# Kernel tuning notes

Measured on AMD Instinct MI355X. Metric: run time of the kernel, lower is better.

## Reference

```python
import jax, jax.numpy as jnp
import numpy as np

T = 1024
HID = 2880
H = 64        # query heads
KVH = 8       # kv heads
G = H // KVH  # GQA group size
D = 64        # head dim
WIN = 128     # sliding window
BASE = 150000.0
INIT_CTX = 4096
SCALING = 32.0
NTK_ALPHA = 1.0
NTK_BETA = 32.0
EPS = 1e-5


def _rope_cache():
    # YaRN-style NTK rope cache (scaling_factor > 1 branch), computed in float32.
    d_half = D // 2
    freq = BASE ** (np.arange(0, D, 2, dtype=np.float64) / D)
    concentration = 0.1 * np.log(SCALING) + 1.0
    low = d_half * np.log(INIT_CTX / (NTK_BETA * 2 * np.pi)) / np.log(BASE)
    high = d_half * np.log(INIT_CTX / (NTK_ALPHA * 2 * np.pi)) / np.log(BASE)
    interpolation = 1.0 / (SCALING * freq)
    extrapolation = 1.0 / freq
    ramp = (np.arange(d_half, dtype=np.float64) - low) / (high - low)
    mask = 1.0 - np.clip(ramp, 0.0, 1.0)
    inv_freq = interpolation * (1.0 - mask) + extrapolation * mask
    t = np.arange(INIT_CTX, dtype=np.float64)
    freqs = np.outer(t, inv_freq)                  # [INIT_CTX, D/2]
    cos = (np.cos(freqs) * concentration).astype(np.float32)
    sin = (np.sin(freqs) * concentration).astype(np.float32)
    return jnp.asarray(cos), jnp.asarray(sin)

_COS, _SIN = _rope_cache()


def _apply_rope(x, cos, sin):
    # x: [T, nh, D], cos/sin: [T, D/2]
    c = cos[:, None, :]
    s = sin[:, None, :]
    x1, x2 = jnp.split(x, 2, axis=-1)
    return jnp.concatenate([x1 * c - x2 * s, x2 * c + x1 * s], axis=-1)


def setup_inputs() -> dict:
    key = jax.random.key(0)
    ks = jax.random.split(key, 8)
    hidden_states = jax.random.normal(ks[0], (T, HID), dtype=jnp.float32)
    positions = jnp.arange(T, dtype=jnp.int32)
    norm_scale = jnp.ones((HID,), dtype=jnp.float32)
    qkv_out = H * D + 2 * KVH * D  # 4096 + 512 + 512
    w_qkv = jax.random.normal(ks[1], (HID, qkv_out), dtype=jnp.float32) * (HID ** -0.5)
    b_qkv = jax.random.normal(ks[2], (qkv_out,), dtype=jnp.float32) * 0.01
    w_out = jax.random.normal(ks[3], (H * D, HID), dtype=jnp.float32) * ((H * D) ** -0.5)
    b_out = jax.random.normal(ks[4], (HID,), dtype=jnp.float32) * 0.01
    sinks = jax.random.normal(ks[5], (H,), dtype=jnp.float32)
    return {"hidden_states": hidden_states, "positions": positions,
            "norm_scale": norm_scale, "w_qkv": w_qkv, "b_qkv": b_qkv,
            "w_out": w_out, "b_out": b_out, "sinks": sinks}


def reference(hidden_states, positions, norm_scale, w_qkv, b_qkv, w_out, b_out, sinks):
    # RMSNorm (fp32 math)
    t = hidden_states
    t = t * jax.lax.rsqrt(jnp.mean(t * t, axis=-1, keepdims=True) + EPS)
    t = t * norm_scale

    # fused QKV projection
    qkv = t @ w_qkv + b_qkv
    q = qkv[:, : H * D].reshape(T, H, D)
    k = qkv[:, H * D: H * D + KVH * D].reshape(T, KVH, D)
    v = qkv[:, H * D + KVH * D:].reshape(T, KVH, D)

    # RoPE
    cos = _COS[positions]
    sin = _SIN[positions]
    q = _apply_rope(q, cos, sin)
    k = _apply_rope(k, cos, sin)

    # GQA attention with sliding window + learned sinks
    qg = q.reshape(T, KVH, G, D)
    scale = D ** -0.5
    scores = jnp.einsum('qhgd,khd->hgqk', qg, k) * scale  # [KVH, G, T, T]
    i = jnp.arange(T)[:, None]
    j = jnp.arange(T)[None, :]
    allowed = (j <= i) & (j > i - WIN)  # causal + sliding window
    scores = jnp.where(allowed, scores, -jnp.inf)
    sink = sinks.reshape(KVH, G)[..., None]  # [KVH, G, 1]
    lse = jnp.logaddexp(jax.nn.logsumexp(scores, axis=-1), sink)  # [KVH, G, T]
    probs = jnp.exp(scores - lse[..., None])  # sink mass not attached to any value
    attn = jnp.einsum('hgqk,khd->qhgd', probs, v).reshape(T, H * D)

    out = attn @ w_out + b_out
    return out + hidden_states
```

## Files before the change

### kernel.cpp

```cpp
#include <hip/hip_runtime.h>
#include <hip/hip_bf16.h>
#include <math.h>

#define T_SEQ 1024
#define HIDD 2880
#define NH   64
#define NKVH 8
#define GQ   8
#define HD   64
#define WIN  128
#define QKV_N 5120
#define QDIM  4096
#define KOFF  4096
#define VOFF  4608
#define NPAD_OUT 3072
#define RMS_EPS 1e-5f
#define Z1 3
#define KS1 960
#define Z2 4
#define KS2 1024
#define P1SZ (T_SEQ * QKV_N)
#define P2SZ (T_SEQ * HIDD)

typedef __attribute__((ext_vector_type(8))) short short8;
typedef __attribute__((ext_vector_type(4))) short s16x4;
typedef __attribute__((ext_vector_type(4))) float floatx4;

__device__ __forceinline__ float bf2f(unsigned short u) {
    unsigned int x = ((unsigned int)u) << 16;
    float f; __builtin_memcpy(&f, &x, 4); return f;
}
__device__ __forceinline__ unsigned short f2bf(float f) {
    unsigned int x; __builtin_memcpy(&x, &f, 4);
    unsigned int r = (x + 0x7fffu + ((x >> 16) & 1u)) >> 16;
    return (unsigned short)r;
}
__device__ __forceinline__ void glds16(const unsigned short* g, unsigned short* l) {
    __builtin_amdgcn_global_load_lds(
        (const __attribute__((address_space(1))) void*)g,
        (__attribute__((address_space(3))) void*)l, 16, 0, 0);
}

__global__ __launch_bounds__(256) void prep_kernel(
    const float* __restrict__ w_qkv, const float* __restrict__ w_out,
    const float* __restrict__ hidden, const float* __restrict__ norm_scale,
    const int* __restrict__ positions,
    unsigned short* __restrict__ bqkvT, unsigned short* __restrict__ boutT,
    unsigned short* __restrict__ xn,
    float* __restrict__ tabc, float* __restrict__ tabs)
{
    __shared__ unsigned short tile[64 * 66];
    __shared__ float red[4];
    int blk = blockIdx.x;
    int t = threadIdx.x;

    if (blk < 6672) {
        const float* in; unsigned short* out; int R, C, bx, by;
        if (blk < 3600) { in = w_qkv; out = bqkvT; R = HIDD; C = QKV_N; bx = blk % 80; by = blk / 80; }
        else { int r = blk - 3600; in = w_out; out = boutT; R = QDIM; C = HIDD; bx = r % 48; by = r / 48; }
        int r0 = by * 64, c0 = bx * 64;
        bool inr = (c0 < C);
#pragma unroll
        for (int p = 0; p < 4; ++p) {
            int row = p * 16 + (t >> 4);
            int col = (t & 15) * 4;
            float4 v = inr ? *(const float4*)&in[(size_t)(r0 + row) * C + c0 + col]
                           : make_float4(0.f, 0.f, 0.f, 0.f);
            unsigned int w0 = (unsigned)f2bf(v.x) | ((unsigned)f2bf(v.y) << 16);
            unsigned int w1 = (unsigned)f2bf(v.z) | ((unsigned)f2bf(v.w) << 16);
            *(unsigned int*)&tile[row * 66 + col]     = w0;
            *(unsigned int*)&tile[row * 66 + col + 2] = w1;
        }
        __syncthreads();
        int oc = t >> 2, ks = (t & 3) * 16;
        unsigned short vbuf[16];
#pragma unroll
        for (int j = 0; j < 16; ++j) vbuf[j] = tile[(ks + j) * 66 + oc];
        unsigned short* dst = &out[(size_t)(c0 + oc) * R + r0 + ks];
        *(uint4*)dst       = *(uint4*)&vbuf[0];
        *(uint4*)(dst + 8) = *(uint4*)&vbuf[8];
    } else if (blk < 7696) {
        int row = blk - 6672;
        const float4* hr4 = (const float4*)(hidden + (size_t)row * HIDD);
        const float4* sc4 = (const float4*)norm_scale;
        float ss = 0.f;
        for (int i = t; i < HIDD / 4; i += 256) {
            float4 v = hr4[i];
            ss += v.x * v.x + v.y * v.y + v.z * v.z + v.w * v.w;
        }
        for (int m = 32; m; m >>= 1) ss += __shfl_xor(ss, m, 64);
        if ((t & 63) == 0) red[t >> 6] = ss;
        __syncthreads();
        float tot = red[0] + red[1] + red[2] + red[3];
        float r = rsqrtf(tot / (float)HIDD + RMS_EPS);
        uint2* xr = (uint2*)(xn + (size_t)row * HIDD);
        for (int i = t; i < HIDD / 4; i += 256) {
            float4 v = hr4[i], s4 = sc4[i];
            unsigned int lo = (unsigned)f2bf(v.x * r * s4.x) | ((unsigned)f2bf(v.y * r * s4.y) << 16);
            unsigned int hi = (unsigned)f2bf(v.z * r * s4.z) | ((unsigned)f2bf(v.w * r * s4.w) << 16);
            uint2 o; o.x = lo; o.y = hi;
            xr[i] = o;
        }
    } else {
        int idx = (blk - 7696) * 256 + t;
        int tt = idx >> 5, i = idx & 31;
        double freq = pow(150000.0, (double)(2 * i) / 64.0);
        double lnbase = log(150000.0);
        double low  = 32.0 * log(4096.0 / (32.0 * 2.0 * M_PI)) / lnbase;
        double high = 32.0 * log(4096.0 / (2.0 * M_PI)) / lnbase;
        double ramp = ((double)i - low) / (high - low);
        double mask = 1.0 - fmin(fmax(ramp, 0.0), 1.0);
        double invf = (1.0 / (32.0 * freq)) * (1.0 - mask) + (1.0 / freq) * mask;
        double conc = 0.1 * log(32.0) + 1.0;
        double ang = (double)positions[tt] * invf;
        tabc[idx] = (float)(cos(ang) * conc);
        tabs[idx] = (float)(sin(ang) * conc);
    }
}


#define SYNCPRE() do { \
    __builtin_amdgcn_s_barrier(); \
    asm volatile("s_waitcnt lgkmcnt(0)"); \
    __builtin_amdgcn_s_setprio(1); \
} while (0)
#define SYNCPOST() do { \
    __builtin_amdgcn_s_setprio(0); \
    __builtin_amdgcn_s_barrier(); \
} while (0)

#define LDA_FRAGS(SLOT, QM) do { \
    const unsigned short* _pa = lds + ((SLOT)*4 + (QM)) * 8192 + rowA * 64; \
    _Pragma("unroll") \
    for (int _t = 0; _t < 4; ++_t) { \
        af[_t][0] = *(const short8*)(_pa + _t * 1024 + sl0); \
        af[_t][1] = *(const short8*)(_pa + _t * 1024 + sl1); \
    } \
} while (0)

#define LDB_FRAGS(SLOT, QN, BF) do { \
    const unsigned short* _pb = lds + ((SLOT)*4 + 2 + (QN)) * 8192 + rowB * 64; \
    _Pragma("unroll") \
    for (int _u = 0; _u < 2; ++_u) { \
        BF[_u][0] = *(const short8*)(_pb + _u * 1024 + sl0); \
        BF[_u][1] = *(const short8*)(_pb + _u * 1024 + sl1); \
    } \
} while (0)

#define MFMA_Q(QM, QN, BF) do { \
    _Pragma("unroll") \
    for (int _t = 0; _t < 4; ++_t) { \
        _Pragma("unroll") \
        for (int _u = 0; _u < 2; ++_u) { \
            floatx4 _c = acc[QM][_t][QN][_u]; \
            _c = __builtin_amdgcn_mfma_f32_16x16x32_bf16(af[_t][0], BF[_u][0], _c, 0, 0, 0); \
            _c = __builtin_amdgcn_mfma_f32_16x16x32_bf16(af[_t][1], BF[_u][1], _c, 0, 0, 0); \
            acc[QM][_t][QN][_u] = _c; \
        } \
    } \
} while (0)

#define STAGE(SLOT, MAT, HALF, GP, GR0, KT) do { \
    unsigned short* _d = lds + ((SLOT)*4 + (MAT)*2 + (HALF)) * 8192 + stdst; \
    const unsigned short* _s = (GP) + (size_t)((GR0) + (HALF)*128 + st_r0) * K + kbeg + (KT)*64 + st_c0; \
    glds16(_s, _d); \
    glds16(_s + (size_t)8 * K, _d + 512); \
} while (0)

template <int NX>
__global__ __launch_bounds__(512, 2) void gemm256_kernel(
    const unsigned short* __restrict__ A, const unsigned short* __restrict__ BT,
    unsigned short* __restrict__ P, int M, int N, int K, int Ks)
{
    __shared__ unsigned short lds[65536];

    int b = blockIdx.x;
    int cpx = (int)gridDim.x >> 3;
    int sid = (b & 7) * cpx + (b >> 3);
    int y = sid & 3;
    int xz = sid >> 2;
    int x = xz % NX, z = xz / NX;
    int m0 = y * 256, n0 = x * 256;
    int kbeg = z * Ks;
    int NT = Ks >> 6;
    int NIT = NT >> 1;

    int tid = threadIdx.x;
    int ln = tid & 63, wv = tid >> 6;
    int l16 = ln & 15, quad = ln >> 4;
    int wm = wv >> 2, wn = wv & 3;
    int e8 = l16 & 7;
    int sl0 = ((quad ^ e8) << 3);
    int sl1 = (((4 + quad) ^ e8) << 3);
    int rowA = wm * 64 + l16;
    int rowB = wn * 32 + l16;
    int st_r0 = (wv << 4) + (ln >> 3);
    int st_c0 = (((ln & 7) ^ ((ln >> 3) & 7)) << 3);
    int stdst = (wv << 10) + (ln << 3);

    short8 af[4][2], b0[2][2], b1[2][2];
    floatx4 acc[2][4][2][2];
#pragma unroll
    for (int qm = 0; qm < 2; ++qm)
#pragma unroll
        for (int t = 0; t < 4; ++t)
#pragma unroll
            for (int qn = 0; qn < 2; ++qn)
#pragma unroll
                for (int u = 0; u < 2; ++u)
                    acc[qm][t][qn][u] = (floatx4){0.f, 0.f, 0.f, 0.f};

    STAGE(0, 0, 0, A,  m0, 0); STAGE(0, 0, 1, A,  m0, 0);
    STAGE(0, 1, 0, BT, n0, 0); STAGE(0, 1, 1, BT, n0, 0);
    STAGE(1, 0, 0, A,  m0, 1); STAGE(1, 1, 0, BT, n0, 1);
    asm volatile("s_waitcnt vmcnt(0)");
    __builtin_amdgcn_s_barrier();

    int a = 0;
    for (int i = 0; i < NIT; ++i, a += 2) {
        bool k2 = (a + 2) < NT, k3 = (a + 3) < NT;
        LDA_FRAGS(0, 0); LDB_FRAGS(0, 0, b0);
        STAGE(1, 1, 1, BT, n0, a + 1); STAGE(1, 0, 1, A, m0, a + 1);
        SYNCPRE(); MFMA_Q(0, 0, b0); SYNCPOST();
        LDB_FRAGS(0, 1, b1);
        SYNCPRE(); MFMA_Q(0, 1, b1); SYNCPOST();
        LDA_FRAGS(0, 1);
        if (k2) STAGE(0, 0, 0, A, m0, a + 2);
        SYNCPRE(); MFMA_Q(1, 0, b0); SYNCPOST();
        if (k2) { STAGE(0, 1, 0, BT, n0, a + 2); asm volatile("s_waitcnt vmcnt(8)"); }
        else    { asm volatile("s_waitcnt vmcnt(4)"); }
        SYNCPRE(); MFMA_Q(1, 1, b1); SYNCPOST();
        LDA_FRAGS(1, 0); LDB_FRAGS(1, 0, b0);
        if (k2) { STAGE(0, 1, 1, BT, n0, a + 2); STAGE(0, 0, 1, A, m0, a + 2);
                  asm volatile("s_waitcnt vmcnt(8)"); }
        else    { asm volatile("s_waitcnt vmcnt(0)"); }
        SYNCPRE(); MFMA_Q(0, 0, b0); SYNCPOST();
        LDB_FRAGS(1, 1, b1);
        SYNCPRE(); MFMA_Q(0, 1, b1); SYNCPOST();
        LDA_FRAGS(1, 1);
        if (k3) STAGE(1, 0, 0, A, m0, a + 3);
        SYNCPRE(); MFMA_Q(1, 0, b0); SYNCPOST();
        if (k3) { STAGE(1, 1, 0, BT, n0, a + 3); asm volatile("s_waitcnt vmcnt(4)"); }
        else    { asm volatile("s_waitcnt vmcnt(0)"); }
        SYNCPRE(); MFMA_Q(1, 1, b1); SYNCPOST();
    }
    if (NT & 1) {
        LDA_FRAGS(0, 0); LDB_FRAGS(0, 0, b0);
        SYNCPRE(); MFMA_Q(0, 0, b0); SYNCPOST();
        LDB_FRAGS(0, 1, b1);
        SYNCPRE(); MFMA_Q(0, 1, b1); SYNCPOST();
        LDA_FRAGS(0, 1);
        SYNCPRE(); MFMA_Q(1, 0, b0); SYNCPOST();
        SYNCPRE(); MFMA_Q(1, 1, b1); SYNCPOST();
    }

    unsigned short* Pz = P + (size_t)z * M * N;
#pragma unroll
    for (int qm = 0; qm < 2; ++qm)
#pragma unroll
        for (int t = 0; t < 4; ++t) {
            int rbase = m0 + qm * 128 + wm * 64 + t * 16 + quad * 4;
#pragma unroll
            for (int qn = 0; qn < 2; ++qn)
#pragma unroll
                for (int u = 0; u < 2; ++u) {
                    int col = n0 + qn * 128 + wn * 32 + u * 16 + l16;
                    if (col < N) {
#pragma unroll
                        for (int r = 0; r < 4; ++r)
                            Pz[(size_t)(rbase + r) * N + col] = f2bf(acc[qm][t][qn][u][r]);
                    }
                }
        }
}

__global__ __launch_bounds__(256) void reduce_out_kernel(
    const unsigned short* __restrict__ P, const float* __restrict__ bias,
    const float* __restrict__ resid, float* __restrict__ out)
{
    int idx = (blockIdx.x * 256 + threadIdx.x) * 4;
    int n = idx % HIDD;
    float4 rv = *(const float4*)(resid + idx);
    float4 bv = *(const float4*)(bias + n);
    float a0 = bv.x + rv.x, a1 = bv.y + rv.y, a2 = bv.z + rv.z, a3 = bv.w + rv.w;
#pragma unroll
    for (int z = 0; z < Z2; ++z) {
        s16x4 p = *(const s16x4*)(P + (size_t)z * P2SZ + idx);
        a0 += bf2f((unsigned short)p[0]);
        a1 += bf2f((unsigned short)p[1]);
        a2 += bf2f((unsigned short)p[2]);
        a3 += bf2f((unsigned short)p[3]);
    }
    float4 ov = {a0, a1, a2, a3};
    *(float4*)(out + idx) = ov;
}

__global__ __launch_bounds__(512) void attn_kernel(
    const unsigned short* __restrict__ P1, const float* __restrict__ b_qkv,
    const float* __restrict__ sinks,
    const float* __restrict__ tabc, const float* __restrict__ tabs,
    unsigned short* __restrict__ attn)
{
    int i0 = blockIdx.x * 16;
    int kh = blockIdx.y;
    int tid = threadIdx.x, lane = tid & 63, g = tid >> 6;
    int quad = lane >> 4, l16 = lane & 15;
    int tile_j0 = i0 - 127;

    __shared__ unsigned short sU[8 * 16 * 168];
    __shared__ unsigned short sVt[64 * 168];
    unsigned short* sK = sU;
    unsigned short* sPw = sU + g * 16 * 168;

    {
        int d = lane, dd = lane & 31;
        float kb1 = b_qkv[KOFF + kh * 64 + d];
        float kb2 = b_qkv[KOFF + kh * 64 + (d ^ 32)];
        float vb  = b_qkv[VOFF + kh * 64 + d];
        for (int it = 0; it < 18; ++it) {
            int s = it * 8 + g;
            int j = tile_j0 + s;
            unsigned short kst = 0, vst = 0;
            if (j >= 0 && j < T_SEQ) {
                size_t ko = (size_t)j * QKV_N + KOFF + kh * 64;
                float x1 = kb1, x2 = kb2, vv = vb;
#pragma unroll
                for (int z = 0; z < Z1; ++z) {
                    const unsigned short* Pz = P1 + (size_t)z * P1SZ;
                    x1 += bf2f(Pz[ko + d]);
                    x2 += bf2f(Pz[ko + (d ^ 32)]);
                    vv += bf2f(Pz[ko + 512 + d]);
                }
                float c = tabc[j * 32 + dd], sn = tabs[j * 32 + dd];
                kst = f2bf((d < 32) ? (x1 * c - x2 * sn) : (x1 * c + x2 * sn));
                vst = f2bf(vv);
            }
            sK[s * 72 + d] = kst;
            sVt[d * 168 + s] = vst;
        }
        sVt[d * 168 + 144 + 2 * g]     = 0;
        sVt[d * 168 + 144 + 2 * g + 1] = 0;
    }

    int qi = i0 + l16;
    int hb = (kh * GQ + g) * 64;
    short8 qa, qb;
    {
        size_t qo = (size_t)qi * QKV_N + hb + quad * 8;
        float x1[8], x2[8];
#pragma unroll
        for (int j = 0; j < 8; ++j) {
            x1[j] = b_qkv[hb + quad * 8 + j];
            x2[j] = b_qkv[hb + quad * 8 + 32 + j];
        }
#pragma unroll
        for (int z = 0; z < Z1; ++z) {
            const unsigned short* Pz = P1 + (size_t)z * P1SZ;
            short8 lo = *(const short8*)(Pz + qo);
            short8 hi = *(const short8*)(Pz + qo + 32);
#pragma unroll
            for (int j = 0; j < 8; ++j) {
                x1[j] += bf2f((unsigned short)lo[j]);
                x2[j] += bf2f((unsigned short)hi[j]);
            }
        }
        const float* cc = tabc + qi * 32 + quad * 8;
        const float* sc = tabs + qi * 32 + quad * 8;
#pragma unroll
        for (int j = 0; j < 8; ++j) {
            float c = cc[j] * 0.125f, sn = sc[j] * 0.125f;
            qa[j] = (short)f2bf(x1[j] * c - x2[j] * sn);
            qb[j] = (short)f2bf(x2[j] * c + x1[j] * sn);
        }
    }
    __syncthreads();

    floatx4 Sc[9];
#pragma unroll
    for (int nt = 0; nt < 9; ++nt) Sc[nt] = (floatx4){0.f, 0.f, 0.f, 0.f};
#pragma unroll
    for (int nt = 0; nt < 9; ++nt) {
        short8 kb0 = *(const short8*)&sK[(nt * 16 + l16) * 72 + quad * 8];
        short8 kb1 = *(const short8*)&sK[(nt * 16 + l16) * 72 + 32 + quad * 8];
        Sc[nt] = __builtin_amdgcn_mfma_f32_16x16x32_bf16(qa, kb0, Sc[nt], 0, 0, 0);
        Sc[nt] = __builtin_amdgcn_mfma_f32_16x16x32_bf16(qb, kb1, Sc[nt], 0, 0, 0);
    }

    int smin = 127 - i0;
    float mx[4], sm[4], inv[4];
#pragma unroll
    for (int r = 0; r < 4; ++r) {
        int qoff = quad * 4 + r;
        int lo = qoff > smin ? qoff : smin;
        int hi = qoff + 127;
        float m = -INFINITY;
#pragma unroll
        for (int nt = 0; nt < 9; ++nt) {
            int s = nt * 16 + l16;
            float v = (s >= lo && s <= hi) ? Sc[nt][r] : -INFINITY;
            Sc[nt][r] = v;
            m = fmaxf(m, v);
        }
        mx[r] = m;
    }
#pragma unroll
    for (int mmask = 1; mmask < 16; mmask <<= 1)
#pragma unroll
        for (int r = 0; r < 4; ++r)
            mx[r] = fmaxf(mx[r], __shfl_xor(mx[r], mmask, 64));
    float sink = sinks[kh * GQ + g];
#pragma unroll
    for (int r = 0; r < 4; ++r) {
        mx[r] = fmaxf(mx[r], sink);
        float s = 0.f;
#pragma unroll
        for (int nt = 0; nt < 9; ++nt) {
            float p = __expf(Sc[nt][r] - mx[r]);
            Sc[nt][r] = p;
            s += p;
        }
        sm[r] = s;
    }
#pragma unroll
    for (int mmask = 1; mmask < 16; mmask <<= 1)
#pragma unroll
        for (int r = 0; r < 4; ++r)
            sm[r] += __shfl_xor(sm[r], mmask, 64);
#pragma unroll
    for (int r = 0; r < 4; ++r)
        inv[r] = 1.f / (sm[r] + __expf(sink - mx[r]));

    __syncthreads();

#pragma unroll
    for (int nt = 0; nt < 9; ++nt)
#pragma unroll
        for (int r = 0; r < 4; ++r)
            sPw[(quad * 4 + r) * 168 + nt * 16 + l16] = f2bf(Sc[nt][r]);
    {
        int q = lane >> 2, so = (lane & 3) * 4;
        *(s16x4*)&sPw[q * 168 + 144 + so] = (s16x4){0, 0, 0, 0};
    }

    floatx4 O[4];
#pragma unroll
    for (int nt = 0; nt < 4; ++nt) O[nt] = (floatx4){0.f, 0.f, 0.f, 0.f};
#pragma unroll
    for (int kt = 0; kt < 5; ++kt) {
        short8 pa = *(const short8*)&sPw[l16 * 168 + kt * 32 + quad * 8];
#pragma unroll
        for (int nt = 0; nt < 4; ++nt) {
            short8 vb = *(const short8*)&sVt[(nt * 16 + l16) * 168 + kt * 32 + quad * 8];
            O[nt] = __builtin_amdgcn_mfma_f32_16x16x32_bf16(pa, vb, O[nt], 0, 0, 0);
        }
    }
#pragma unroll
    for (int nt = 0; nt < 4; ++nt)
#pragma unroll
        for (int r = 0; r < 4; ++r) {
            int q = quad * 4 + r;
            attn[(size_t)(i0 + q) * QDIM + (kh * GQ + g) * 64 + nt * 16 + l16] =
                f2bf(O[nt][r] * inv[r]);
        }
}

extern "C" void kernel_launch(void* const* d_in, const int* in_sizes, int n_in,
                              void* d_out, int out_size, void* d_ws, size_t ws_size,
                              hipStream_t stream)
{
    const float* hidden     = (const float*)d_in[0];
    const int*   positions  = (const int*)d_in[1];
    const float* norm_scale = (const float*)d_in[2];
    const float* w_qkv      = (const float*)d_in[3];
    const float* b_qkv      = (const float*)d_in[4];
    const float* w_out      = (const float*)d_in[5];
    const float* b_out      = (const float*)d_in[6];
    const float* sinks      = (const float*)d_in[7];
    float* out = (float*)d_out;

    char* ws = (char*)d_ws;
    float*          tabc  = (float*)ws;
    float*          tabs  = (float*)(ws + 131072);
    unsigned short* boutT = (unsigned short*)(ws + 262144);
    unsigned short* xn    = (unsigned short*)(ws + 25427968);
    unsigned short* bqkvT = (unsigned short*)(ws + 31326208);
    unsigned short* P1    = (unsigned short*)(ws + 60817408);
    unsigned short* attnb = (unsigned short*)(ws + 25427968);
    unsigned short* P2    = (unsigned short*)(ws + 60817408);

    prep_kernel<<<7824, 256, 0, stream>>>(
        w_qkv, w_out, hidden, norm_scale, positions, bqkvT, boutT, xn, tabc, tabs);
    gemm256_kernel<20><<<4 * 20 * Z1, 512, 0, stream>>>(
        xn, bqkvT, P1, T_SEQ, QKV_N, HIDD, KS1);
    attn_kernel<<<dim3(T_SEQ / 16, NKVH), 512, 0, stream>>>(
        P1, b_qkv, sinks, tabc, tabs, attnb);
    gemm256_kernel<12><<<4 * 12 * Z2, 512, 0, stream>>>(
        attnb, boutT, P2, T_SEQ, HIDD, QDIM, KS2);
    reduce_out_kernel<<<2880, 256, 0, stream>>>(P2, b_out, hidden, out);
}
```

Before: 254.9 us.

## Enlarge weight-transpose tiles, rebalance out-proj split-K, cheapen RoPE trig

The weight convert-and-transpose path in the prep kernel now uses tall tiles: 320 rows for w_qkv and 256 rows for w_out. Each block writes longer contiguous bf16 runs, and the launch shrinks from 7824 to 2640 blocks. The output-projection GEMM split-K changes from 4×1024 to 5×832, with the last slice clamped to the remaining K. RoPE tables now do a double-precision range reduction and then call float cosf/sinf instead of double cos/sin. The risks are that 832/64 gives an odd tile count per slice, which the pipelined loop may not handle, and that an extra split-K partial adds workspace traffic and work for the reduction.

Result: slower. 264.2 us (+3.6%).

```diff
diff --git a/kernel.cpp b/kernel.cpp
--- a/kernel.cpp
+++ b/kernel.cpp
@@ -17,8 +17,8 @@
 #define RMS_EPS 1e-5f
 #define Z1 3
 #define KS1 960
-#define Z2 4
-#define KS2 1024
+#define Z2 5
+#define KS2 832
 #define P1SZ (T_SEQ * QKV_N)
 #define P2SZ (T_SEQ * HIDD)
 
@@ -49,38 +49,62 @@
     unsigned short* __restrict__ xn,
     float* __restrict__ tabc, float* __restrict__ tabs)
 {
-    __shared__ unsigned short tile[64 * 66];
+    __shared__ unsigned short tile[320 * 66];
     __shared__ float red[4];
     int blk = blockIdx.x;
     int t = threadIdx.x;
 
-    if (blk < 6672) {
-        const float* in; unsigned short* out; int R, C, bx, by;
-        if (blk < 3600) { in = w_qkv; out = bqkvT; R = HIDD; C = QKV_N; bx = blk % 80; by = blk / 80; }
-        else { int r = blk - 3600; in = w_out; out = boutT; R = QDIM; C = HIDD; bx = r % 48; by = r / 48; }
-        int r0 = by * 64, c0 = bx * 64;
-        bool inr = (c0 < C);
-#pragma unroll
-        for (int p = 0; p < 4; ++p) {
-            int row = p * 16 + (t >> 4);
-            int col = (t & 15) * 4;
-            float4 v = inr ? *(const float4*)&in[(size_t)(r0 + row) * C + c0 + col]
+    if (blk < 720) {
+        int bx = blk % 80, by = blk / 80;
+        int r0 = by * 320, c0 = bx * 64;
+        int rrow = t >> 4, rcol = (t & 15) * 4;
+#pragma unroll
+        for (int p = 0; p < 20; ++p) {
+            int row = p * 16 + rrow;
+            float4 v = *(const float4*)&w_qkv[(size_t)(r0 + row) * QKV_N + c0 + rcol];
+            unsigned int w0 = (unsigned)f2bf(v.x) | ((unsigned)f2bf(v.y) << 16);
+            unsigned int w1 = (unsigned)f2bf(v.z) | ((unsigned)f2bf(v.w) << 16);
+            *(unsigned int*)&tile[row * 66 + rcol]     = w0;
+            *(unsigned int*)&tile[row * 66 + rcol + 2] = w1;
+        }
+        __syncthreads();
+        int col = t >> 2, seg = t & 3;
+        unsigned short* dst = &bqkvT[(size_t)(c0 + col) * HIDD + r0 + seg * 80];
+#pragma unroll
+        for (int p = 0; p < 10; ++p) {
+            unsigned short vb[8];
+#pragma unroll
+            for (int j = 0; j < 8; ++j) vb[j] = tile[(seg * 80 + p * 8 + j) * 66 + col];
+            *(uint4*)(dst + p * 8) = *(uint4*)vb;
+        }
+    } else if (blk < 1488) {
+        int r = blk - 720;
+        int bx = r % 48, by = r / 48;
+        int r0 = by * 256, c0 = bx * 64;
+        bool inr = (c0 < HIDD);
+        int rrow = t >> 4, rcol = (t & 15) * 4;
+#pragma unroll
+        for (int p = 0; p < 16; ++p) {
+            int row = p * 16 + rrow;
+            float4 v = inr ? *(const float4*)&w_out[(size_t)(r0 + row) * HIDD + c0 + rcol]
                            : make_float4(0.f, 0.f, 0.f, 0.f);
             unsigned int w0 = (unsigned)f2bf(v.x) | ((unsigned)f2bf(v.y) << 16);
             unsigned int w1 = (unsigned)f2bf(v.z) | ((unsigned)f2bf(v.w) << 16);
-            *(unsigned int*)&tile[row * 66 + col]     = w0;
-            *(unsigned int*)&tile[row * 66 + col + 2] = w1;
+            *(unsigned int*)&tile[row * 66 + rcol]     = w0;
+            *(unsigned int*)&tile[row * 66 + rcol + 2] = w1;
         }
         __syncthreads();
-        int oc = t >> 2, ks = (t & 3) * 16;
-        unsigned short vbuf[16];
-#pragma unroll
-        for (int j = 0; j < 16; ++j) vbuf[j] = tile[(ks + j) * 66 + oc];
-        unsigned short* dst = &out[(size_t)(c0 + oc) * R + r0 + ks];
-        *(uint4*)dst       = *(uint4*)&vbuf[0];
-        *(uint4*)(dst + 8) = *(uint4*)&vbuf[8];
-    } else if (blk < 7696) {
-        int row = blk - 6672;
+        int col = t >> 2, seg = t & 3;
+        unsigned short* dst = &boutT[(size_t)(c0 + col) * QDIM + r0 + seg * 64];
+#pragma unroll
+        for (int p = 0; p < 8; ++p) {
+            unsigned short vb[8];
+#pragma unroll
+            for (int j = 0; j < 8; ++j) vb[j] = tile[(seg * 64 + p * 8 + j) * 66 + col];
+            *(uint4*)(dst + p * 8) = *(uint4*)vb;
+        }
+    } else if (blk < 2512) {
+        int row = blk - 1488;
         const float4* hr4 = (const float4*)(hidden + (size_t)row * HIDD);
         const float4* sc4 = (const float4*)norm_scale;
         float ss = 0.f;
@@ -102,7 +126,7 @@
             xr[i] = o;
         }
     } else {
-        int idx = (blk - 7696) * 256 + t;
+        int idx = (blk - 2512) * 256 + t;
         int tt = idx >> 5, i = idx & 31;
         double freq = pow(150000.0, (double)(2 * i) / 64.0);
         double lnbase = log(150000.0);
@@ -113,8 +137,10 @@
         double invf = (1.0 / (32.0 * freq)) * (1.0 - mask) + (1.0 / freq) * mask;
         double conc = 0.1 * log(32.0) + 1.0;
         double ang = (double)positions[tt] * invf;
-        tabc[idx] = (float)(cos(ang) * conc);
-        tabs[idx] = (float)(sin(ang) * conc);
+        double tw = floor(ang * (1.0 / (2.0 * M_PI)));
+        float ar = (float)(ang - tw * (2.0 * M_PI));
+        tabc[idx] = cosf(ar) * (float)conc;
+        tabs[idx] = sinf(ar) * (float)conc;
     }
 }
 
@@ -182,7 +208,8 @@
     int x = xz % NX, z = xz / NX;
     int m0 = y * 256, n0 = x * 256;
     int kbeg = z * Ks;
-    int NT = Ks >> 6;
+    int kslice = K - kbeg; if (kslice > Ks) kslice = Ks;
+    int NT = kslice >> 6;
     int NIT = NT >> 1;
 
     int tid = threadIdx.x;
@@ -488,7 +515,7 @@
     unsigned short* attnb = (unsigned short*)(ws + 25427968);
     unsigned short* P2    = (unsigned short*)(ws + 60817408);
 
-    prep_kernel<<<7824, 256, 0, stream>>>(
+    prep_kernel<<<2640, 256, 0, stream>>>(
         w_qkv, w_out, hidden, norm_scale, positions, bqkvT, boutT, xn, tabc, tabs);
     gemm256_kernel<20><<<4 * 20 * Z1, 512, 0, stream>>>(
         xn, bqkvT, P1, T_SEQ, QKV_N, HIDD, KS1);
```
